# Optimization experiments

Measured on AMD Instinct MI355X. Metric: run time of the kernel, lower is better.

Reference implementation:

```python
import jax, jax.numpy as jnp
import numpy as np

B, S, D, H = 2, 2048, 1024, 16
HD = D // H  # head_dim = 64


def setup_inputs() -> dict:
    key = jax.random.key(0)
    ks = jax.random.split(key, 8)
    scale = 0.02
    return {
        "hidden_states": jax.random.normal(ks[0], (B, S, D), dtype=jnp.float32),
        "attn_mask": jnp.zeros((B, 1, 1, S), dtype=jnp.float32),  # additive mask
        "Wq": jax.random.normal(ks[1], (D, D), dtype=jnp.float32) * scale,
        "bq": jnp.zeros((D,), dtype=jnp.float32),
        "Wk": jax.random.normal(ks[2], (D, D), dtype=jnp.float32) * scale,
        "bk": jnp.zeros((D,), dtype=jnp.float32),
        "Wv": jax.random.normal(ks[3], (D, D), dtype=jnp.float32) * scale,
        "bv": jnp.zeros((D,), dtype=jnp.float32),
    }


def reference(hidden_states, attn_mask, Wq, bq, Wk, bk, Wv, bv):
    # QKV projections: nn.Linear(dim, dim) -> x @ W.T + b
    def proj(x, W, b):
        y = jnp.einsum("bsd,ed->bse", x, W) + b
        # split heads: [B, S, D] -> [B, H, S, HD]
        return y.reshape(B, S, H, HD).transpose(0, 2, 1, 3)

    q = proj(hidden_states, Wq, bq)
    k = proj(hidden_states, Wk, bk)
    v = proj(hidden_states, Wv, bv)

    # scaled dot-product scores + additive mask (hack_torch_trace(scores, mask))
    scores = jnp.einsum("bhqd,bhkd->bhqk", q, k) / jnp.sqrt(jnp.float32(HD))
    scores = scores + attn_mask  # broadcast [B,1,1,S]
    probs = jax.nn.softmax(scores, axis=-1)  # attn dropout = identity (eval)

    ctx = jnp.einsum("bhqk,bhkd->bhqd", probs, v)
    # merge heads: [B, H, S, HD] -> [B, S, D]
    attn_outputs = ctx.transpose(0, 2, 1, 3).reshape(B, S, D)
    return attn_outputs
```

## Files before the change

kernel.cpp:

```cpp
#include <hip/hip_runtime.h>
#include <hip/hip_bf16.h>
#include <math.h>


typedef __bf16 bf16_t;
typedef __attribute__((ext_vector_type(8))) __bf16 bf16x8;
typedef __attribute__((ext_vector_type(4))) __bf16 bf16x4;
typedef __attribute__((ext_vector_type(4))) float f32x4;

#define B_  2
#define S_  2048
#define D_  1024
#define H_  16
#define HD_ 64
#define M_  (B_ * S_)
#define K_  D_
#define NT_ (S_ / 64)
#define LOG2E 1.44269504f
#define CS_Q (0.125f * LOG2E)

#if __has_builtin(__builtin_amdgcn_exp2f)
#define EXP2F(x) __builtin_amdgcn_exp2f(x)
#else
#define EXP2F(x) exp2f(x)
#endif

__device__ __forceinline__ f32x4 mfma16x16x32(bf16x8 a, bf16x8 b, f32x4 c) {
    return __builtin_amdgcn_mfma_f32_16x16x32_bf16(a, b, c, 0, 0, 0);
}

__device__ __forceinline__ void gload_lds16(const bf16_t* g, bf16_t* l) {
    __builtin_amdgcn_global_load_lds(
        (const __attribute__((address_space(1))) void*)g,
        (__attribute__((address_space(3))) void*)l,
        16, 0, 0);
}

__global__ void cvt_all(const float* __restrict__ hs, const float* __restrict__ wq,
                        const float* __restrict__ wk, const float* __restrict__ wv,
                        const float* __restrict__ mask,
                        bf16_t* __restrict__ Xb, bf16_t* __restrict__ Wb3,
                        float* __restrict__ wfp, bf16_t* __restrict__ wfb) {
    const int i = blockIdx.x * blockDim.x + threadIdx.x;
    if (i >= 1835008) {
        const int off = i - 1835008;
        if (off < 1024) {
            float4 v = ((const float4*)mask)[off];
            float4 w4;
            w4.x = exp2f(v.x * LOG2E); w4.y = exp2f(v.y * LOG2E);
            w4.z = exp2f(v.z * LOG2E); w4.w = exp2f(v.w * LOG2E);
            ((float4*)wfp)[off] = w4;
            const int k4 = off * 4;
            const int bb = k4 >> 11, k = k4 & 2047;
            const int t  = k >> 6,  kt = k & 63;
            const int nb = kt >> 4, kgf = (kt >> 2) & 3;
            bf16x4 wb4;
            wb4[0] = (bf16_t)w4.x; wb4[1] = (bf16_t)w4.y;
            wb4[2] = (bf16_t)w4.z; wb4[3] = (bf16_t)w4.w;
            *(bf16x4*)&wfb[(((size_t)bb * 32 + t) * 4 + kgf) * 16 + nb * 4] = wb4;
        }
        return;
    }
    const float* src; bf16_t* dst; int off;
    if (i < 1048576)      { src = hs; dst = Xb;            off = i; }
    else if (i < 1310720) { src = wq; dst = Wb3;           off = i - 1048576; }
    else if (i < 1572864) { src = wk; dst = Wb3 + 1048576; off = i - 1310720; }
    else                  { src = wv; dst = Wb3 + 2097152; off = i - 1572864; }
    float4 v = ((const float4*)src)[off];
    bf16x4 o;
    o[0] = (bf16_t)v.x; o[1] = (bf16_t)v.y;
    o[2] = (bf16_t)v.z; o[3] = (bf16_t)v.w;
    ((bf16x4*)dst)[off] = o;
}

__global__ __launch_bounds__(256, 4)
void gemm_qkv(const bf16_t* __restrict__ Xb, const bf16_t* __restrict__ Wb3,
              const float* __restrict__ bq, const float* __restrict__ bk,
              const float* __restrict__ bv,
              const float* __restrict__ wfp,
              bf16_t* __restrict__ Qo, bf16_t* __restrict__ Ko,
              bf16_t* __restrict__ Vf) {
    __shared__ bf16_t smem[2][8192];
    const int z = blockIdx.z;
    const bf16_t* Wb = Wb3 + (size_t)z * (D_ * K_);
    const float* bias = (z == 0) ? bq : (z == 1) ? bk : bv;

    const int tid  = threadIdx.x;
    const int lane = tid & 63;
    const int w    = tid >> 6;
    const int wr   = w >> 1, wc = w & 1;
    const int m0   = blockIdx.y * 128;
    const int n0   = blockIdx.x * 128;

    f32x4 acc[4][4];
    const f32x4 fzero = {0.f, 0.f, 0.f, 0.f};
#pragma unroll
    for (int i = 0; i < 4; i++)
#pragma unroll
        for (int j = 0; j < 4; j++) acc[i][j] = fzero;

    const int koff = (lane >> 4) * 8;

    auto stage = [&](int k0, int buf) {
#pragma unroll
        for (int i = 0; i < 4; i++) {
            const int chunk  = w * 4 + i;
            const int byteoff = chunk * 1024 + lane * 16;
            bf16_t* ldst = &smem[buf][chunk * 512];
            const bf16_t* gsrc;
            if (byteoff < 8192) {
                int row = byteoff >> 6;
                int col = (byteoff & 63) >> 1;
                gsrc = Xb + (size_t)(m0 + row) * K_ + k0 + col;
            } else {
                int bo  = byteoff - 8192;
                int row = bo >> 6;
                int col = (bo & 63) >> 1;
                gsrc = Wb + (size_t)(n0 + row) * K_ + k0 + col;
            }
            gload_lds16(gsrc, ldst);
        }
    };

    stage(0, 0);
    __syncthreads();

    for (int kk = 0; kk < K_ / 32; ++kk) {
        const int cur = kk & 1;
        if (kk + 1 < K_ / 32) stage((kk + 1) * 32, cur ^ 1);

        bf16x8 af[4], bfr[4];
#pragma unroll
        for (int m = 0; m < 4; m++) {
            int row = wr * 64 + m * 16 + (lane & 15);
            af[m] = *(const bf16x8*)&smem[cur][row * 32 + koff];
        }
#pragma unroll
        for (int n = 0; n < 4; n++) {
            int row = wc * 64 + n * 16 + (lane & 15);
            bfr[n] = *(const bf16x8*)&smem[cur][4096 + row * 32 + koff];
        }
#pragma unroll
        for (int m = 0; m < 4; m++)
#pragma unroll
            for (int n = 0; n < 4; n++)
                acc[m][n] = mfma16x16x32(af[m], bfr[n], acc[m][n]);

        __syncthreads();
    }

#pragma unroll
    for (int m = 0; m < 4; m++) {
        const int gm    = m0 + wr * 64 + m * 16 + ((lane >> 4) << 2);
        const int bidx  = gm >> 11;
        const int sbase = gm & 2047;
#pragma unroll
        for (int n = 0; n < 4; n++) {
            const int gn = n0 + wc * 64 + n * 16 + (lane & 15);
            const int h  = gn >> 6, hd = gn & 63;
            const float bias_v = bias[gn];
            const size_t bh = (size_t)bidx * H_ + h;
            if (z == 2) {
                const int t   = sbase >> 6, k0i = sbase & 63;
                const int nb  = k0i >> 4, kgf = (k0i >> 2) & 3;
                const int db  = hd >> 4,  lqf = hd & 15;
                const float4 w4 = *(const float4*)&wfp[bidx * S_ + sbase];
                bf16x4 pack;
                pack[0] = (bf16_t)((acc[m][n][0] + bias_v) * w4.x);
                pack[1] = (bf16_t)((acc[m][n][1] + bias_v) * w4.y);
                pack[2] = (bf16_t)((acc[m][n][2] + bias_v) * w4.z);
                pack[3] = (bf16_t)((acc[m][n][3] + bias_v) * w4.w);
                bf16_t* dst = Vf + ((bh * 32 + t) * 4 + db) * 1024 +
                    (kgf * 16 + lqf) * 16 + nb * 4;
                *(bf16x4*)dst = pack;
            } else if (z == 0) {
#pragma unroll
                for (int j = 0; j < 4; j++) {
                    float y = (acc[m][n][j] + bias_v) * CS_Q;
                    Qo[(bh * S_ + sbase + j) * HD_ + hd] = (bf16_t)y;
                }
            } else {
#pragma unroll
                for (int j = 0; j < 4; j++) {
                    float y = acc[m][n][j] + bias_v;
                    Ko[(bh * S_ + sbase + j) * HD_ + hd] = (bf16_t)y;
                }
            }
        }
    }
}

__global__ __launch_bounds__(256, 2)
void attn_fwd(const bf16_t* __restrict__ Qb, const bf16_t* __restrict__ Kb,
              const bf16_t* __restrict__ Vf, const bf16_t* __restrict__ Wfb,
              float* __restrict__ out) {
    const int flat = blockIdx.x;
    const int xcd  = flat & 7;
    const int idx  = flat >> 3;
    const int bh   = xcd * 4 + (idx >> 4);
    const int qt   = idx & 15;
    const int b    = bh >> 4;
    const int h    = bh & 15;

    const int tid  = threadIdx.x, lane = tid & 63, w = tid >> 6;

    const bf16_t* Qh = Qb + (size_t)bh * S_ * HD_;
    const bf16_t* Kh = Kb + (size_t)bh * S_ * HD_;
    const bf16_t* Vh = Vf + (size_t)bh * 32 * 4096;
    const bf16_t* Wh = Wfb + (size_t)b * 32 * 64;

    __shared__ char ShBuf[16384];

    const int lq   = lane & 15;
    const int kg   = lane >> 4;
    const int koff = kg * 8;
    const int rsub = lane >> 3;
    const int csl8 = (lane & 7) * 8;

    auto stageK = [&](int kv0, int buf) {
        bf16_t* base = (bf16_t*)(ShBuf + buf * 8192);
#pragma unroll
        for (int i = 0; i < 2; i++) {
            const int c = w * 2 + i;
            bf16_t* ldst = base + c * 512;
            const int cel = csl8 ^ (rsub * 8);
            const bf16_t* gsrc = Kh + (size_t)(kv0 + c * 8 + rsub) * HD_ + cel;
            gload_lds16(gsrc, ldst);
        }
    };

    const int qbase = qt * 128 + w * 32;
    bf16x8 qf0[2], qf1[2];
#pragma unroll
    for (int s = 0; s < 2; s++) {
        const bf16_t* qr = Qh + (size_t)(qbase + s * 16 + lq) * HD_;
        qf0[s] = *(const bf16x8*)(qr + koff);
        qf1[s] = *(const bf16x8*)(qr + 32 + koff);
    }

    const f32x4 fzero = {0.f, 0.f, 0.f, 0.f};
    f32x4 of[2][4];
    f32x4 of_l[2];
#pragma unroll
    for (int s = 0; s < 2; s++) {
        of_l[s] = fzero;
#pragma unroll
        for (int i = 0; i < 4; i++) of[s][i] = fzero;
    }

    const int rdsw = (lq & 7) << 4;

    bf16x8 va[4], vb[4], wf0, wf1;
    {
        const bf16_t* Vt_ = Vh;
#pragma unroll
        for (int db = 0; db < 4; db++) {
            const bf16_t* vp = Vt_ + db * 1024 + lane * 16;
            va[db] = *(const bf16x8*)(vp);
            vb[db] = *(const bf16x8*)(vp + 8);
        }
        wf0 = *(const bf16x8*)(Wh + kg * 16);
        wf1 = *(const bf16x8*)(Wh + kg * 16 + 8);
    }
    stageK(0, 0);
    __syncthreads();

    for (int t = 0; t < NT_; ++t) {
        const int cur = t & 1;

        bf16x8 nva[4], nvb[4], nwf0, nwf1;
        if (t + 1 < NT_) {
            const bf16_t* Vn = Vh + (size_t)(t + 1) * 4096;
#pragma unroll
            for (int db = 0; db < 4; db++) {
                const bf16_t* vp = Vn + db * 1024 + lane * 16;
                nva[db] = *(const bf16x8*)(vp);
                nvb[db] = *(const bf16x8*)(vp + 8);
            }
            const bf16_t* wp = Wh + (size_t)(t + 1) * 64 + kg * 16;
            nwf0 = *(const bf16x8*)(wp);
            nwf1 = *(const bf16x8*)(wp + 8);
            stageK((t + 1) * 64, cur ^ 1);
        }

        const char* KB = ShBuf + cur * 8192;

        bf16x8 kf0[4], kf1[4];
#pragma unroll
        for (int nb = 0; nb < 4; nb++) {
            const char* kr = KB + (nb * 16 + lq) * 128;
            kf0[nb] = *(const bf16x8*)(kr + ((kg * 16) ^ rdsw));
            kf1[nb] = *(const bf16x8*)(kr + ((64 + kg * 16) ^ rdsw));
        }

        f32x4 sc[2][4];
#pragma unroll
        for (int s = 0; s < 2; s++)
#pragma unroll
            for (int nb = 0; nb < 4; nb++) {
                f32x4 tacc = fzero;
                tacc = mfma16x16x32(kf0[nb], qf0[s], tacc);
                tacc = mfma16x16x32(kf1[nb], qf1[s], tacc);
                sc[s][nb] = tacc;
            }

        bf16x8 pa0[2], pa1[2];
#pragma unroll
        for (int s = 0; s < 2; s++)
#pragma unroll
            for (int nb = 0; nb < 4; nb++)
#pragma unroll
                for (int j = 0; j < 4; j++) {
                    float p = EXP2F(sc[s][nb][j]);
                    const int e = (nb & 1) * 4 + j;
                    if (nb < 2) pa0[s][e] = (bf16_t)p; else pa1[s][e] = (bf16_t)p;
                }

#pragma unroll
        for (int s = 0; s < 2; s++) {
#pragma unroll
            for (int db = 0; db < 4; db++) {
                of[s][db] = mfma16x16x32(pa0[s], va[db], of[s][db]);
                of[s][db] = mfma16x16x32(pa1[s], vb[db], of[s][db]);
            }
            of_l[s] = mfma16x16x32(pa0[s], wf0, of_l[s]);
            of_l[s] = mfma16x16x32(pa1[s], wf1, of_l[s]);
        }

        __syncthreads();

        if (t + 1 < NT_) {
#pragma unroll
            for (int db = 0; db < 4; db++) { va[db] = nva[db]; vb[db] = nvb[db]; }
            wf0 = nwf0; wf1 = nwf1;
        }
    }

#pragma unroll
    for (int s = 0; s < 2; s++) {
        float inv[4];
#pragma unroll
        for (int j = 0; j < 4; j++) inv[j] = 1.0f / of_l[s][j];
#pragma unroll
        for (int db = 0; db < 4; db++) {
            const int d = h * HD_ + db * 16 + lq;
#pragma unroll
            for (int j = 0; j < 4; j++) {
                const int row = qbase + s * 16 + kg * 4 + j;
                out[((size_t)b * S_ + row) * D_ + d] = of[s][db][j] * inv[j];
            }
        }
    }
}

extern "C" void kernel_launch(void* const* d_in, const int* in_sizes, int n_in,
                              void* d_out, int out_size, void* d_ws, size_t ws_size,
                              hipStream_t stream) {
    const float* hs   = (const float*)d_in[0];
    const float* mask = (const float*)d_in[1];
    const float* Wq   = (const float*)d_in[2];
    const float* bq   = (const float*)d_in[3];
    const float* Wk   = (const float*)d_in[4];
    const float* bk   = (const float*)d_in[5];
    const float* Wv   = (const float*)d_in[6];
    const float* bv   = (const float*)d_in[7];
    float* out = (float*)d_out;

    char* ws = (char*)d_ws;
    bf16_t* Xb  = (bf16_t*)(ws);
    bf16_t* Wb3 = (bf16_t*)(ws + 8388608);
    bf16_t* Qb  = (bf16_t*)(ws + 14680064);
    bf16_t* Kb  = (bf16_t*)(ws + 23068672);
    bf16_t* Vfr = (bf16_t*)(ws + 31457280);
    float*  wfp = (float*)(ws + 39845888);
    bf16_t* wfb = (bf16_t*)(ws + 39862272);

    cvt_all<<<7172, 256, 0, stream>>>(hs, Wq, Wk, Wv, mask, Xb, Wb3, wfp, wfb);

    dim3 ggrid(D_ / 128, M_ / 128, 3);
    gemm_qkv<<<ggrid, 256, 0, stream>>>(Xb, Wb3, bq, bk, bv, wfp, Qb, Kb, Vfr);

    attn_fwd<<<512, 256, 0, stream>>>(Qb, Kb, Vfr, wfb, out);
}
```

Measured before the change: 87.54 us.

## Software-pipeline attention loop: overlap next QK^T with previous tile's softmax-PV

Restructures the key-tile loop so the exp and PV/rowsum MFMAs for tile t-1 are issued alongside the QK^T MFMAs for tile t, with a three-stage register rotation for V and W fragments. The epilogue drains the final tile after the loop. The aim is to hide exp latency and MFMA dependency stalls by interleaving independent work. In exchange it holds more V and W fragments live at once, which raises register pressure and could lower occupancy.

```diff
diff --git a/kernel.cpp b/kernel.cpp
--- a/kernel.cpp
+++ b/kernel.cpp
@@ -250,39 +250,28 @@
 
     const int rdsw = (lq & 7) << 4;
 
-    bf16x8 va[4], vb[4], wf0, wf1;
+    bf16x8 vA[4], vB[4], vC[4], wA0, wA1, wB0, wB1, wC0, wC1;
     {
         const bf16_t* Vt_ = Vh;
 #pragma unroll
         for (int db = 0; db < 4; db++) {
             const bf16_t* vp = Vt_ + db * 1024 + lane * 16;
-            va[db] = *(const bf16x8*)(vp);
-            vb[db] = *(const bf16x8*)(vp + 8);
-        }
-        wf0 = *(const bf16x8*)(Wh + kg * 16);
-        wf1 = *(const bf16x8*)(Wh + kg * 16 + 8);
-    }
+            vB[db] = *(const bf16x8*)(vp);
+            vC[db] = *(const bf16x8*)(vp + 8);
+        }
+        wB0 = *(const bf16x8*)(Wh + kg * 16);
+        wB1 = *(const bf16x8*)(Wh + kg * 16 + 8);
+    }
+    bf16x8 vLoA[4], vHiA[4], vLoB[4], vHiB[4], vLoC[4], vHiC[4];
+#pragma unroll
+    for (int db = 0; db < 4; db++) { vLoB[db] = vB[db]; vHiB[db] = vC[db]; }
     stageK(0, 0);
     __syncthreads();
 
+    f32x4 sc[2][4];
+
     for (int t = 0; t < NT_; ++t) {
         const int cur = t & 1;
-
-        bf16x8 nva[4], nvb[4], nwf0, nwf1;
-        if (t + 1 < NT_) {
-            const bf16_t* Vn = Vh + (size_t)(t + 1) * 4096;
-#pragma unroll
-            for (int db = 0; db < 4; db++) {
-                const bf16_t* vp = Vn + db * 1024 + lane * 16;
-                nva[db] = *(const bf16x8*)(vp);
-                nvb[db] = *(const bf16x8*)(vp + 8);
-            }
-            const bf16_t* wp = Wh + (size_t)(t + 1) * 64 + kg * 16;
-            nwf0 = *(const bf16x8*)(wp);
-            nwf1 = *(const bf16x8*)(wp + 8);
-            stageK((t + 1) * 64, cur ^ 1);
-        }
-
         const char* KB = ShBuf + cur * 8192;
 
         bf16x8 kf0[4], kf1[4];
@@ -293,7 +282,31 @@
             kf1[nb] = *(const bf16x8*)(kr + ((64 + kg * 16) ^ rdsw));
         }
 
-        f32x4 sc[2][4];
+        if (t > 0) {
+            bf16x8 pa0[2], pa1[2];
+#pragma unroll
+            for (int s = 0; s < 2; s++)
+#pragma unroll
+                for (int nb = 0; nb < 4; nb++)
+#pragma unroll
+                    for (int j = 0; j < 4; j++) {
+                        float p = EXP2F(sc[s][nb][j]);
+                        const int e = (nb & 1) * 4 + j;
+                        if (nb < 2) pa0[s][e] = (bf16_t)p;
+                        else        pa1[s][e] = (bf16_t)p;
+                    }
+#pragma unroll
+            for (int s = 0; s < 2; s++) {
+#pragma unroll
+                for (int db = 0; db < 4; db++) {
+                    of[s][db] = mfma16x16x32(pa0[s], vLoA[db], of[s][db]);
+                    of[s][db] = mfma16x16x32(pa1[s], vHiA[db], of[s][db]);
+                }
+                of_l[s] = mfma16x16x32(pa0[s], wA0, of_l[s]);
+                of_l[s] = mfma16x16x32(pa1[s], wA1, of_l[s]);
+            }
+        }
+
 #pragma unroll
         for (int s = 0; s < 2; s++)
 #pragma unroll
@@ -304,6 +317,32 @@
                 sc[s][nb] = tacc;
             }
 
+        if (t + 1 < NT_) {
+            const bf16_t* Vn = Vh + (size_t)(t + 1) * 4096;
+#pragma unroll
+            for (int db = 0; db < 4; db++) {
+                const bf16_t* vp = Vn + db * 1024 + lane * 16;
+                vLoC[db] = *(const bf16x8*)(vp);
+                vHiC[db] = *(const bf16x8*)(vp + 8);
+            }
+            const bf16_t* wp = Wh + (size_t)(t + 1) * 64 + kg * 16;
+            wC0 = *(const bf16x8*)(wp);
+            wC1 = *(const bf16x8*)(wp + 8);
+            stageK((t + 1) * 64, cur ^ 1);
+        }
+
+        __syncthreads();
+
+#pragma unroll
+        for (int db = 0; db < 4; db++) {
+            vLoA[db] = vLoB[db]; vHiA[db] = vHiB[db];
+            vLoB[db] = vLoC[db]; vHiB[db] = vHiC[db];
+        }
+        wA0 = wB0; wA1 = wB1;
+        wB0 = wC0; wB1 = wC1;
+    }
+
+    {
         bf16x8 pa0[2], pa1[2];
 #pragma unroll
         for (int s = 0; s < 2; s++)
@@ -313,26 +352,18 @@
                 for (int j = 0; j < 4; j++) {
                     float p = EXP2F(sc[s][nb][j]);
                     const int e = (nb & 1) * 4 + j;
-                    if (nb < 2) pa0[s][e] = (bf16_t)p; else pa1[s][e] = (bf16_t)p;
+                    if (nb < 2) pa0[s][e] = (bf16_t)p;
+                    else        pa1[s][e] = (bf16_t)p;
                 }
-
 #pragma unroll
         for (int s = 0; s < 2; s++) {
 #pragma unroll
             for (int db = 0; db < 4; db++) {
-                of[s][db] = mfma16x16x32(pa0[s], va[db], of[s][db]);
-                of[s][db] = mfma16x16x32(pa1[s], vb[db], of[s][db]);
-            }
-            of_l[s] = mfma16x16x32(pa0[s], wf0, of_l[s]);
-            of_l[s] = mfma16x16x32(pa1[s], wf1, of_l[s]);
-        }
-
-        __syncthreads();
-
-        if (t + 1 < NT_) {
-#pragma unroll
-            for (int db = 0; db < 4; db++) { va[db] = nva[db]; vb[db] = nvb[db]; }
-            wf0 = nwf0; wf1 = nwf1;
+                of[s][db] = mfma16x16x32(pa0[s], vLoA[db], of[s][db]);
+                of[s][db] = mfma16x16x32(pa1[s], vHiA[db], of[s][db]);
+            }
+            of_l[s] = mfma16x16x32(pa0[s], wA0, of_l[s]);
+            of_l[s] = mfma16x16x32(pa1[s], wA1, of_l[s]);
         }
     }
 
```

Result: no change. 86.49 us (-1.2%).
